# Kernel tuning notes

Measured on AMD Instinct MI355X. Metric: run time of the kernel, lower is better.

Reference implementation:

```python
import jax, jax.numpy as jnp
import numpy as np

VOCAB = 32000
EMBED = 512
HIDDEN = 1024
MAX_VOCAB = 33000
MAX_LEN = 128
BATCH = 64


def setup_inputs() -> dict:
    key = jax.random.key(0)
    ks = jax.random.split(key, 20)
    s = 0.02
    H, E, L, V = HIDDEN, EMBED, MAX_LEN, VOCAB
    return {
        "input_tok": jax.random.randint(ks[0], (BATCH,), 0, V, dtype=jnp.int64 if jax.config.jax_enable_x64 else jnp.int32),
        "hidden": jax.random.normal(ks[1], (1, BATCH, H), jnp.float32),
        "encoder_outputs": jax.random.normal(ks[2], (BATCH, L, H), jnp.float32),
        "input_seq": jax.random.randint(ks[3], (BATCH, L), 0, V, dtype=jnp.int64 if jax.config.jax_enable_x64 else jnp.int32),
        "pre_prob": jax.random.uniform(ks[4], (BATCH, L), jnp.float32),
        "emb": jax.random.normal(ks[5], (V, E), jnp.float32) * s,
        "attn_W": jax.random.normal(ks[6], (L, H + E), jnp.float32) * s,
        "attn_b": jnp.zeros((L,), jnp.float32),
        "comb_W": jax.random.normal(ks[7], (H, H + E), jnp.float32) * s,
        "comb_b": jnp.zeros((H,), jnp.float32),
        "W_ih": jax.random.normal(ks[8], (3 * H, 2 * H), jnp.float32) * s,
        "W_hh": jax.random.normal(ks[9], (3 * H, H), jnp.float32) * s,
        "b_ih": jnp.zeros((3 * H,), jnp.float32),
        "b_hh": jnp.zeros((3 * H,), jnp.float32),
        "Wo_W": jax.random.normal(ks[10], (V, H), jnp.float32) * s,
        "Wo_b": jnp.zeros((V,), jnp.float32),
        "Wc_W": jax.random.normal(ks[11], (H, H), jnp.float32) * s,
        "Wc_b": jnp.zeros((H,), jnp.float32),
    }


def _decoder_step(input_tok, hidden, encoder_outputs, input_seq, pre_prob,
                  emb, attn_W, attn_b, comb_W, comb_b,
                  W_ih, W_hh, b_ih, b_hh, Wo_W, Wo_b, Wc_W, Wc_b):
    B = encoder_outputs.shape[0]
    H = hidden.shape[-1]
    V = Wo_W.shape[0]
    # selective read: mask where previous output token matches source tokens
    sel = (input_tok[:, None] == input_seq).astype(pre_prob.dtype) * pre_prob  # [B,L]
    # torch does encoder_outputs.long().float() -> truncation toward zero
    sel_reading = jnp.einsum('bl,blh->bh', sel, jnp.trunc(encoder_outputs))  # [B,H]

    embedded = emb[input_tok]  # [B,E] (dropout is identity in eval)
    h = hidden[0]  # [B,H]

    a = jnp.concatenate([embedded, h], axis=1) @ attn_W.T + attn_b  # [B,L]
    attn_weights = jax.nn.softmax(a, axis=1)
    attn_applied = jnp.einsum('bl,blh->bh', attn_weights, encoder_outputs)  # [B,H]

    out = jnp.concatenate([embedded, attn_applied], axis=1) @ comb_W.T + comb_b
    out = jax.nn.relu(out)  # [B,H]

    gru_in = jnp.concatenate([out, sel_reading], axis=1)  # [B,2H]
    gi = gru_in @ W_ih.T + b_ih  # [B,3H]
    gh = h @ W_hh.T + b_hh       # [B,3H]
    i_r, i_z, i_n = jnp.split(gi, 3, axis=1)
    h_r, h_z, h_n = jnp.split(gh, 3, axis=1)
    r = jax.nn.sigmoid(i_r + h_r)
    z = jax.nn.sigmoid(i_z + h_z)
    n = jnp.tanh(i_n + r * h_n)
    h_new = (1.0 - z) * n + z * h  # [B,H]

    score_g = h_new @ Wo_W.T + Wo_b  # [B,V]
    score_c = jnp.tanh(encoder_outputs @ Wc_W.T + Wc_b)  # [B,L,H]
    score_c = jnp.einsum('blh,bh->bl', score_c, h_new)   # [B,L]

    score = jax.nn.softmax(jnp.concatenate([score_g, score_c], axis=1), axis=1)
    prob_g = score[:, :V]
    prob_c = score[:, V:]  # [B,L]

    output1 = jnp.concatenate(
        [prob_g, jnp.zeros((B, MAX_VOCAB - V), prob_g.dtype)], axis=1)  # [B,MAX_VOCAB]
    # bmm(prob_c, one_hot(input_seq)) == scatter-add of copy probs onto vocab ids
    b_idx = jnp.arange(B)[:, None]
    output1 = output1.at[b_idx, input_seq].add(prob_c)
    output1 = jnp.where(output1 == 0, 1e-9, output1)
    output1 = output1.at[:, 2].set(1e-9)
    output1 = jnp.log(output1)
    return output1, h_new[None], attn_weights, prob_c


def reference(input_tok, hidden, encoder_outputs, input_seq, pre_prob,
              emb, attn_W, attn_b, comb_W, comb_b,
              W_ih, W_hh, b_ih, b_hh, Wo_W, Wo_b, Wc_W, Wc_b):
    return _decoder_step(input_tok, hidden, encoder_outputs, input_seq, pre_prob,
                         emb, attn_W, attn_b, comb_W, comb_b,
                         W_ih, W_hh, b_ih, b_hh, Wo_W, Wo_b, Wc_W, Wc_b)
```

## Files before the change

kernel.cpp:

```cpp
#include <hip/hip_runtime.h>
#include <math.h>

#define BB 64
#define LL 128
#define HH 1024
#define EE 512
#define VV 32000
#define MAXV 33000

typedef float f32x4 __attribute__((ext_vector_type(4)));
typedef short bf16x8 __attribute__((ext_vector_type(8)));
typedef unsigned u32x4 __attribute__((ext_vector_type(4)));

__device__ __forceinline__ void gload_lds16(const void* g, void* l) {
    __builtin_amdgcn_global_load_lds((const __attribute__((address_space(1))) void*)g,
                                     (__attribute__((address_space(3))) void*)l, 16, 0, 0);
}

__device__ __forceinline__ unsigned short f2bf(float f) {
    unsigned u = __float_as_uint(f);
    return (unsigned short)((u + 0x7fffu + ((u >> 16) & 1u)) >> 16);
}

__device__ __forceinline__ unsigned pkbf(float a, float b) {
    unsigned r;
    asm("v_cvt_pk_bf16_f32 %0, %1, %2" : "=v"(r) : "v"(a), "v"(b));
    return r;
}

__device__ __forceinline__ float fexp(float x) { return __expf(x); }
__device__ __forceinline__ float flog(float x) { return __logf(x); }
__device__ __forceinline__ float ftanh(float x) { return 1.f - 2.f / (1.f + __expf(2.f * x)); }

__device__ __forceinline__ void smerge(float& m, float& s, float m2, float s2) {
    float nm = fmaxf(m, m2);
    s = s * fexp(m - nm) + s2 * fexp(m2 - nm);
    m = nm;
}

#define N_ENC4 2097152
__global__ void setup2(const float* __restrict__ enc, unsigned short* __restrict__ encB,
                       const float* __restrict__ WcW, unsigned short* __restrict__ WcB,
                       const int* __restrict__ tok, const float* __restrict__ hidden,
                       const float* __restrict__ emb, unsigned short* __restrict__ xaB,
                       const float* __restrict__ attnb, const float* __restrict__ combb,
                       const float* __restrict__ bih, const float* __restrict__ bhh,
                       float* __restrict__ aT, float* __restrict__ gruOutF,
                       float* __restrict__ giT, float* __restrict__ ghT,
                       float* __restrict__ zeros, float* __restrict__ out1) {
    int idx = blockIdx.x * 256 + threadIdx.x;
    if (idx < N_ENC4) {
        float4 v = ((const float4*)enc)[idx];
        ushort4 o;
        o.x = f2bf(v.x); o.y = f2bf(v.y); o.z = f2bf(v.z); o.w = f2bf(v.w);
        ((ushort4*)encB)[idx] = o;
        return;
    }
    idx -= N_ENC4;
    if (idx < 262144) {
        float4 v = ((const float4*)WcW)[idx];
        ushort4 o;
        o.x = f2bf(v.x); o.y = f2bf(v.y); o.z = f2bf(v.z); o.w = f2bf(v.w);
        ((ushort4*)WcB)[idx] = o;
        return;
    }
    idx -= 262144;
    if (idx < 98304) {
        int b = idx / 1536, k = idx % 1536;
        float v = (k < EE) ? emb[tok[b] * EE + k] : hidden[b * HH + (k - EE)];
        xaB[b * 1536 + k] = f2bf(v);
        return;
    }
    idx -= 98304;
    if (idx < 8192) { aT[idx] = attnb[idx >> 6]; return; }
    idx -= 8192;
    if (idx < 65536) { gruOutF[idx] = combb[idx >> 6]; return; }
    idx -= 65536;
    if (idx < 196608) { giT[idx] = bih[idx >> 6]; return; }
    idx -= 196608;
    if (idx < 196608) { ghT[idx] = bhh[idx >> 6]; return; }
    idx -= 196608;
    if (idx < 139264) { zeros[idx] = 0.f; return; }
    idx -= 139264;
    int b = idx / 8000, q = idx % 8000;
    ((float4*)(out1 + (size_t)b * MAXV))[q] = (float4){0.f, 0.f, 0.f, 0.f};
}

template <int DIRECT, int MI>
__device__ __forceinline__ void mgemm_body(int bid,
        const float* __restrict__ W, const float* __restrict__ bias,
        const unsigned short* __restrict__ xA, int sA,
        const unsigned short* __restrict__ xB, int sB, int K1,
        int K, int Kc, int splitk, float* __restrict__ out) {
    int tid = threadIdx.x, w = tid >> 6, lane = tid & 63;
    int rb = bid / splitk, kseg = bid - rb * splitk;
    int r0 = rb * (MI * 64), kb0 = kseg * Kc;
    int lr = lane & 15, lk = lane >> 4;
    int nt = Kc >> 6;
    f32x4 acc[MI][4];
#pragma unroll
    for (int mi = 0; mi < MI; ++mi)
#pragma unroll
        for (int nf = 0; nf < 4; ++nf) acc[mi][nf] = (f32x4){0.f, 0.f, 0.f, 0.f};
    const float* Wr[MI];
#pragma unroll
    for (int mi = 0; mi < MI; ++mi)
        Wr[mi] = W + (size_t)(r0 + w * (MI * 16) + mi * 16 + lr) * K;

    for (int t = 0; t < nt; ++t) {
        int kb = kb0 + t * 64;
        bf16x8 bfr[2][4];
#pragma unroll
        for (int ks = 0; ks < 2; ++ks)
#pragma unroll
            for (int nf = 0; nf < 4; ++nf) {
                int bcol = nf * 16 + lr;
                int kg = kb + ks * 32 + lk * 8;
                const unsigned short* xp = (kg < K1) ? (xA + bcol * sA + kg)
                                                     : (xB + bcol * sB + (kg - K1));
                bfr[ks][nf] = *(const bf16x8*)xp;
            }
        bf16x8 afr[MI][2];
#pragma unroll
        for (int mi = 0; mi < MI; ++mi)
#pragma unroll
            for (int ks = 0; ks < 2; ++ks) {
                const float* wp = Wr[mi] + kb + ks * 32 + lk * 8;
                float4 w0 = *(const float4*)wp;
                float4 w1 = *(const float4*)(wp + 4);
                union { u32x4 u; bf16x8 h; } cv;
                cv.u[0] = pkbf(w0.x, w0.y); cv.u[1] = pkbf(w0.z, w0.w);
                cv.u[2] = pkbf(w1.x, w1.y); cv.u[3] = pkbf(w1.z, w1.w);
                afr[mi][ks] = cv.h;
            }
#pragma unroll
        for (int ks = 0; ks < 2; ++ks)
#pragma unroll
            for (int mi = 0; mi < MI; ++mi)
#pragma unroll
                for (int nf = 0; nf < 4; ++nf)
                    acc[mi][nf] = __builtin_amdgcn_mfma_f32_16x16x32_bf16(
                        afr[mi][ks], bfr[ks][nf], acc[mi][nf], 0, 0, 0);
    }
#pragma unroll
    for (int mi = 0; mi < MI; ++mi)
#pragma unroll
        for (int nf = 0; nf < 4; ++nf)
#pragma unroll
            for (int reg = 0; reg < 4; ++reg) {
                int r = r0 + w * (MI * 16) + mi * 16 + lk * 4 + reg;
                int bcol = nf * 16 + lr;
                float v = acc[mi][nf][reg];
                if (DIRECT) out[r * 64 + bcol] = v + bias[r];
                else atomicAdd(&out[r * 64 + bcol], v);
            }
}

template <int DIRECT, int MI>
__global__ __launch_bounds__(256) void mgemm(
        const float* __restrict__ W, const float* __restrict__ bias,
        const unsigned short* __restrict__ xA, int sA,
        const unsigned short* __restrict__ xB, int sB, int K1,
        int K, int Kc, int splitk, float* __restrict__ out) {
    mgemm_body<DIRECT, MI>(blockIdx.x, W, bias, xA, sA, xB, sB, K1, K, Kc, splitk, out);
}

__global__ __launch_bounds__(256) void gru2(
        const float* __restrict__ Wih, const float* __restrict__ Whh,
        const unsigned short* __restrict__ gruInB, const unsigned short* __restrict__ xaB512,
        float* __restrict__ giT, float* __restrict__ ghT) {
    const float* W; const unsigned short* x; int s, K1, K, Kc; float* out; int bid;
    if (blockIdx.x < 192) { W = Wih; x = gruInB; s = 2048; K1 = 2048; K = 2048; Kc = 256; out = giT; bid = blockIdx.x; }
    else                  { W = Whh; x = xaB512; s = 1536; K1 = 1024; K = 1024; Kc = 128; out = ghT; bid = blockIdx.x - 192; }
    mgemm_body<0, 2>(bid, W, nullptr, x, s, x, s, K1, K, Kc, 8, out);
}

__global__ __launch_bounds__(256) void k2_softmax_enc(
        const float* __restrict__ aT, const int* __restrict__ tok, const int* __restrict__ seq,
        const float* __restrict__ pprob, const float* __restrict__ enc,
        float* __restrict__ ap4T, float* __restrict__ gruSelF, float* __restrict__ out3) {
    int b = blockIdx.x, lc = blockIdx.y, t = threadIdx.x;
    __shared__ float red[256];
    __shared__ float w_s[16], sel_s[16];
    float av = (t < LL) ? aT[t * 64 + b] : -1e30f;
    red[t] = av; __syncthreads();
    for (int s = 128; s > 0; s >>= 1) { if (t < s) red[t] = fmaxf(red[t], red[t + s]); __syncthreads(); }
    float m = red[0]; __syncthreads();
    float e = (t < LL) ? fexp(av - m) : 0.f;
    red[t] = e; __syncthreads();
    for (int s = 128; s > 0; s >>= 1) { if (t < s) red[t] += red[t + s]; __syncthreads(); }
    float Z = red[0]; __syncthreads();
    if (t < LL) {
        float wv = e / Z;
        if (lc == 0) out3[b * LL + t] = wv;
        int l0 = lc * 16;
        if (t >= l0 && t < l0 + 16) {
            w_s[t - l0] = wv;
            sel_s[t - l0] = (seq[b * LL + t] == tok[b]) ? pprob[b * LL + t] : 0.f;
        }
    }
    __syncthreads();
    float accA[4] = {0.f,0.f,0.f,0.f}, accS[4] = {0.f,0.f,0.f,0.f};
    const float* encb = enc + (size_t)b * LL * HH + (size_t)lc * 16 * HH;
    for (int l = 0; l < 16; ++l) {
        float wl = w_s[l], sl = sel_s[l];
#pragma unroll
        for (int i = 0; i < 4; ++i) {
            float ev = encb[l * HH + t + i * 256];
            accA[i] += wl * ev;
            accS[i] += sl * truncf(ev);
        }
    }
#pragma unroll
    for (int i = 0; i < 4; ++i) {
        int h = t + i * 256;
        atomicAdd(&ap4T[(h >> 2) * 256 + b * 4 + (h & 3)], accA[i]);
        atomicAdd(&gruSelF[(h >> 2) * 256 + b * 4 + (h & 3)], accS[i]);
    }
}

__global__ void cvt_ap(const float* __restrict__ ap4T, unsigned short* __restrict__ apB) {
    int tid = blockIdx.x * 256 + threadIdx.x;
    int b = tid & 63, kq = tid >> 6;
    float4 v = *(const float4*)&ap4T[kq * 256 + b * 4];
    ushort4 o;
    o.x = f2bf(v.x); o.y = f2bf(v.y); o.z = f2bf(v.z); o.w = f2bf(v.w);
    *(ushort4*)&apB[b * 1024 + kq * 4] = o;
}

__global__ void cvt_gruIn(const float* __restrict__ gruOutF, const float* __restrict__ gruSelF,
                          unsigned short* __restrict__ gruInB) {
    int tid = blockIdx.x * 256 + threadIdx.x;
    int b = tid & 63, kq = tid >> 6;
    float4 v;
    if (kq < 256) {
        int k = kq * 4;
        v.x = fmaxf(gruOutF[(k + 0) * 64 + b], 0.f);
        v.y = fmaxf(gruOutF[(k + 1) * 64 + b], 0.f);
        v.z = fmaxf(gruOutF[(k + 2) * 64 + b], 0.f);
        v.w = fmaxf(gruOutF[(k + 3) * 64 + b], 0.f);
    } else {
        v = *(const float4*)&gruSelF[(kq - 256) * 256 + b * 4];
    }
    ushort4 o;
    o.x = f2bf(v.x); o.y = f2bf(v.y); o.z = f2bf(v.z); o.w = f2bf(v.w);
    *(ushort4*)&gruInB[b * 2048 + kq * 4] = o;
}

__global__ void k5_gates(const float* __restrict__ giT, const float* __restrict__ ghT,
                         const float* __restrict__ hidden, float* __restrict__ hn4T,
                         unsigned short* __restrict__ hnB, float* __restrict__ out2) {
    int idx = blockIdx.x * 256 + threadIdx.x;
    int r = idx >> 6, b = idx & 63;
    float ir = giT[r * 64 + b], iz = giT[(HH + r) * 64 + b], in_ = giT[(2 * HH + r) * 64 + b];
    float hr = ghT[r * 64 + b], hz = ghT[(HH + r) * 64 + b], hn = ghT[(2 * HH + r) * 64 + b];
    float rr = 1.f / (1.f + fexp(-(ir + hr)));
    float zz = 1.f / (1.f + fexp(-(iz + hz)));
    float nn = ftanh(in_ + rr * hn);
    float hprev = hidden[b * HH + r];
    float hnew = (1.f - zz) * nn + zz * hprev;
    hn4T[(r >> 2) * 256 + b * 4 + (r & 3)] = hnew;
    hnB[b * 1024 + r] = f2bf(hnew);
    out2[b * HH + r] = hnew;
}

__global__ __launch_bounds__(256) void wow_f1(
        const float* __restrict__ WoW, const float* __restrict__ Wob,
        const unsigned short* __restrict__ hnB, float* __restrict__ sgT,
        float* __restrict__ partMt, float* __restrict__ partSt) {
    __shared__ float pm_s[4 * 64], ps_s[4 * 64];
    int tid = threadIdx.x, w = tid >> 6, lane = tid & 63;
    int lr = lane & 15, lk = lane >> 4;
    int r0 = blockIdx.x * 64;
    f32x4 acc[4];
#pragma unroll
    for (int nf = 0; nf < 4; ++nf) acc[nf] = (f32x4){0.f, 0.f, 0.f, 0.f};
    const float* Wr = WoW + (size_t)(r0 + w * 16 + lr) * HH;
    for (int t = 0; t < 16; ++t) {
        int kb = t * 64;
        bf16x8 bfr[2][4];
#pragma unroll
        for (int ks = 0; ks < 2; ++ks)
#pragma unroll
            for (int nf = 0; nf < 4; ++nf)
                bfr[ks][nf] = *(const bf16x8*)(hnB + (nf * 16 + lr) * 1024 + kb + ks * 32 + lk * 8);
        bf16x8 afr[2];
#pragma unroll
        for (int ks = 0; ks < 2; ++ks) {
            const float* wp = Wr + kb + ks * 32 + lk * 8;
            float4 w0 = *(const float4*)wp;
            float4 w1 = *(const float4*)(wp + 4);
            union { u32x4 u; bf16x8 h; } cv;
            cv.u[0] = pkbf(w0.x, w0.y); cv.u[1] = pkbf(w0.z, w0.w);
            cv.u[2] = pkbf(w1.x, w1.y); cv.u[3] = pkbf(w1.z, w1.w);
            afr[ks] = cv.h;
        }
#pragma unroll
        for (int ks = 0; ks < 2; ++ks)
#pragma unroll
            for (int nf = 0; nf < 4; ++nf)
                acc[nf] = __builtin_amdgcn_mfma_f32_16x16x32_bf16(afr[ks], bfr[ks][nf], acc[nf], 0, 0, 0);
    }
#pragma unroll
    for (int nf = 0; nf < 4; ++nf) {
        int bcol = nf * 16 + lr;
        float m = -1e30f, s = 0.f;
#pragma unroll
        for (int reg = 0; reg < 4; ++reg) {
            int r = r0 + w * 16 + lk * 4 + reg;
            float v = acc[nf][reg] + Wob[r];
            sgT[r * 64 + bcol] = v;
            float nm = fmaxf(m, v);
            s = s * fexp(m - nm) + fexp(v - nm);
            m = nm;
        }
#pragma unroll
        for (int d = 16; d <= 32; d <<= 1) {
            float om = __shfl_xor(m, d), os = __shfl_xor(s, d);
            smerge(m, s, om, os);
        }
        if (lk == 0) { pm_s[w * 64 + bcol] = m; ps_s[w * 64 + bcol] = s; }
    }
    __syncthreads();
    if (tid < 64) {
        float m = pm_s[tid], s = ps_s[tid];
        smerge(m, s, pm_s[64 + tid], ps_s[64 + tid]);
        smerge(m, s, pm_s[128 + tid], ps_s[128 + tid]);
        smerge(m, s, pm_s[192 + tid], ps_s[192 + tid]);
        partMt[tid * 512 + blockIdx.x] = m;
        partSt[tid * 512 + blockIdx.x] = s;
    }
}

__global__ __launch_bounds__(256) void k7_mfma(const unsigned short* __restrict__ encB,
        const unsigned short* __restrict__ WcB, const float* __restrict__ Wcb,
        const float* __restrict__ hn4T, float* __restrict__ sc) {
    __shared__ __align__(16) unsigned short As[128 * 64];
    __shared__ __align__(16) unsigned short Bs[128 * 64];
    __shared__ float h_s[128], bias_s[128];
    int tid = threadIdx.x, w = tid >> 6, lane = tid & 63;
    int wm = w >> 1, wn = w & 1;
    int bid = blockIdx.x;
    int swz = (bid & 7) * 64 + (bid >> 3);
    int mt = swz >> 3, nt = swz & 7;
    int m0 = mt * 128, n0 = nt * 128;
    if (tid < 128) {
        int n = n0 + tid;
        bias_s[tid] = Wcb[n];
        h_s[tid] = hn4T[(n >> 2) * 256 + mt * 4 + (n & 3)];
    }
    f32x4 acc[4][4];
#pragma unroll
    for (int mi = 0; mi < 4; ++mi)
#pragma unroll
        for (int ni = 0; ni < 4; ++ni) acc[mi][ni] = (f32x4){0.f, 0.f, 0.f, 0.f};

    for (int kt = 0; kt < 16; ++kt) {
        __syncthreads();
#pragma unroll
        for (int i = 0; i < 4; ++i) {
            int c = i * 256 + tid;
            int row = c >> 3, cc = c & 7;
            int lc2 = cc ^ (row & 7);
            gload_lds16(encB + (size_t)(m0 + row) * HH + kt * 64 + lc2 * 8,
                        (char*)As + (i * 256 + w * 64) * 16);
        }
#pragma unroll
        for (int i = 0; i < 4; ++i) {
            int c = i * 256 + tid;
            int row = c >> 3, cc = c & 7;
            int lc2 = cc ^ (row & 7);
            gload_lds16(WcB + (size_t)(n0 + row) * HH + kt * 64 + lc2 * 8,
                        (char*)Bs + (i * 256 + w * 64) * 16);
        }
        asm volatile("s_waitcnt vmcnt(0)");
        __syncthreads();
#pragma unroll
        for (int ks = 0; ks < 2; ++ks) {
            bf16x8 af[4], bf[4];
#pragma unroll
            for (int mi = 0; mi < 4; ++mi) {
                int rr = wm * 64 + mi * 16 + (lane & 15);
                int lkk = ks * 4 + (lane >> 4);
                af[mi] = *(const bf16x8*)((const char*)As + rr * 128 + ((lkk ^ (rr & 7)) * 16));
            }
#pragma unroll
            for (int ni = 0; ni < 4; ++ni) {
                int rr = wn * 64 + ni * 16 + (lane & 15);
                int lkk = ks * 4 + (lane >> 4);
                bf[ni] = *(const bf16x8*)((const char*)Bs + rr * 128 + ((lkk ^ (rr & 7)) * 16));
            }
#pragma unroll
            for (int mi = 0; mi < 4; ++mi)
#pragma unroll
                for (int ni = 0; ni < 4; ++ni)
                    acc[mi][ni] = __builtin_amdgcn_mfma_f32_16x16x32_bf16(af[mi], bf[ni], acc[mi][ni], 0, 0, 0);
        }
    }
    float rs[16];
#pragma unroll
    for (int z = 0; z < 16; ++z) rs[z] = 0.f;
#pragma unroll
    for (int ni = 0; ni < 4; ++ni) {
        int nl = wn * 64 + ni * 16 + (lane & 15);
        float hv = h_s[nl], bv = bias_s[nl];
#pragma unroll
        for (int mi = 0; mi < 4; ++mi)
#pragma unroll
            for (int reg = 0; reg < 4; ++reg)
                rs[mi * 4 + reg] += ftanh(acc[mi][ni][reg] + bv) * hv;
    }
#pragma unroll
    for (int z = 0; z < 16; ++z) {
        float v = rs[z];
        v += __shfl_xor(v, 1); v += __shfl_xor(v, 2);
        v += __shfl_xor(v, 4); v += __shfl_xor(v, 8);
        rs[z] = v;
    }
    if ((lane & 15) == 0) {
        int g = lane >> 4;
#pragma unroll
        for (int mi = 0; mi < 4; ++mi)
#pragma unroll
            for (int reg = 0; reg < 4; ++reg)
                atomicAdd(&sc[mt * LL + wm * 64 + mi * 16 + g * 4 + reg], rs[mi * 4 + reg]);
    }
}

__global__ __launch_bounds__(256) void f1c_final(const float* __restrict__ partMt,
        const float* __restrict__ partSt, const float* __restrict__ sc,
        const int* __restrict__ seq, float* __restrict__ Mb, float* __restrict__ Zb,
        float* __restrict__ out4, float* __restrict__ out1) {
    int b = blockIdx.x, t = threadIdx.x;
    __shared__ float mred[256], sred[256];
    float m = -1e30f, s = 0.f;
    for (int w = t; w < 500; w += 256)
        smerge(m, s, partMt[b * 512 + w], partSt[b * 512 + w]);
    if (t < 128) smerge(m, s, sc[b * LL + t], 1.0f);
    mred[t] = m; sred[t] = s; __syncthreads();
    for (int st = 128; st > 0; st >>= 1) {
        if (t < st) {
            float mm = mred[t], ss = sred[t];
            smerge(mm, ss, mred[t + st], sred[t + st]);
            mred[t] = mm; sred[t] = ss;
        }
        __syncthreads();
    }
    float M = mred[0], Z = sred[0];
    if (t == 0) { Mb[b] = M; Zb[b] = Z; }
    if (t < 128) {
        float p = fexp(sc[b * LL + t] - M) / Z;
        out4[b * LL + t] = p;
        atomicAdd(&out1[(size_t)b * MAXV + seq[b * LL + t]], p);
    }
}

__global__ void f2f4_final(const float* __restrict__ sgT, const float* __restrict__ Mb,
                           const float* __restrict__ Zb, float* __restrict__ out1) {
    int b = blockIdx.y;
    int v = blockIdx.x * 256 + threadIdx.x;
    if (v >= MAXV) return;
    float val = 0.f;
    if (v < VV) {
        float scat = out1[(size_t)b * MAXV + v];
        val = fexp(sgT[v * 64 + b] - Mb[b]) / Zb[b] + scat;
    }
    if (v == 2 || val == 0.f) val = 1e-9f;
    out1[(size_t)b * MAXV + v] = flog(val);
}

extern "C" void kernel_launch(void* const* d_in, const int* in_sizes, int n_in,
                              void* d_out, int out_size, void* d_ws, size_t ws_size,
                              hipStream_t stream) {
    (void)in_sizes; (void)n_in; (void)out_size; (void)ws_size;
    const int*   tok    = (const int*)  d_in[0];
    const float* hidden = (const float*)d_in[1];
    const float* enc    = (const float*)d_in[2];
    const int*   seq    = (const int*)  d_in[3];
    const float* pprob  = (const float*)d_in[4];
    const float* emb    = (const float*)d_in[5];
    const float* attnW  = (const float*)d_in[6];
    const float* attnb  = (const float*)d_in[7];
    const float* combW  = (const float*)d_in[8];
    const float* combb  = (const float*)d_in[9];
    const float* Wih    = (const float*)d_in[10];
    const float* Whh    = (const float*)d_in[11];
    const float* bih    = (const float*)d_in[12];
    const float* bhh    = (const float*)d_in[13];
    const float* WoW    = (const float*)d_in[14];
    const float* Wob    = (const float*)d_in[15];
    const float* WcW    = (const float*)d_in[16];
    const float* Wcb    = (const float*)d_in[17];

    float* out1 = (float*)d_out;
    float* out2 = out1 + (size_t)BB * MAXV;
    float* out3 = out2 + BB * HH;
    float* out4 = out3 + BB * LL;

    float* ws      = (float*)d_ws;
    float* aT      = ws;
    float* ap4T    = ws + 8192;
    float* gruSelF = ws + 73728;
    float* sc      = ws + 139264;
    float* gruOutF = ws + 147456;
    float* giT     = ws + 212992;
    float* ghT     = ws + 409600;
    float* hn4T    = ws + 606208;
    float* sgT     = ws + 671744;
    float* partMt  = ws + 2719744;
    float* partSt  = ws + 2752512;
    float* Mb      = ws + 2785280;
    float* Zb      = ws + 2785344;
    unsigned short* encB = (unsigned short*)(ws + 2785408);
    unsigned short* WcB  = encB + 8388608;
    unsigned short* hnB  = (unsigned short*)(ws + 7504000);
    unsigned short* xaB    = (unsigned short*)sgT;
    unsigned short* apB    = (unsigned short*)(ws + 720896);
    unsigned short* gruInB = (unsigned short*)(ws + 753664);

    setup2       <<<13968, 256, 0, stream>>>(enc, encB, WcW, WcB, tok, hidden, emb, xaB,
                                             attnb, combb, bih, bhh,
                                             aT, gruOutF, giT, ghT, ap4T, out1);
    mgemm<0,2>   <<<12, 256, 0, stream>>>(attnW, nullptr, xaB, 1536, xaB, 1536, 1536, 1536, 128, 12, aT);
    k2_softmax_enc<<<dim3(64, 8), 256, 0, stream>>>(aT, tok, seq, pprob, enc, ap4T, gruSelF, out3);
    cvt_ap       <<<64, 256, 0, stream>>>(ap4T, apB);
    mgemm<0,2>   <<<96, 256, 0, stream>>>(combW, nullptr, xaB, 1536, apB, 1024, 512, 1536, 128, 12, gruOutF);
    cvt_gruIn    <<<128, 256, 0, stream>>>(gruOutF, gruSelF, gruInB);
    gru2         <<<384, 256, 0, stream>>>(Wih, Whh, gruInB, xaB + 512, giT, ghT);
    k5_gates     <<<256, 256, 0, stream>>>(giT, ghT, hidden, hn4T, hnB, out2);
    wow_f1       <<<500, 256, 0, stream>>>(WoW, Wob, hnB, sgT, partMt, partSt);
    k7_mfma      <<<512, 256, 0, stream>>>(encB, WcB, Wcb, hn4T, sc);
    f1c_final    <<<64, 256, 0, stream>>>(partMt, partSt, sc, seq, Mb, Zb, out4, out1);
    f2f4_final   <<<dim3(129, 64), 256, 0, stream>>>(sgT, Mb, Zb, out1);
}
```

Baseline: 174.4 us.

## Split Wo GEMM K across warps and double block count with register prefetch

The vocab-projection kernel now gives each block 32 rows instead of 64. Its four warps are split into two row groups by two K halves, and the K-half partials are reduced through shared memory. That doubles the grid to 1000 blocks. The loop also prefetches the next fp32 weight chunk into registers before converting and issuing MFMAs, to hide global-load latency on the 131 MB weight stream. The cost is an extra LDS reduction, twice as many softmax partials for the final kernel to merge, and a shifted workspace layout.

Result: slower. 179.9 us (+3.2%).

```diff
diff --git a/kernel.cpp b/kernel.cpp
--- a/kernel.cpp
+++ b/kernel.cpp
@@ -268,67 +268,84 @@
         const float* __restrict__ WoW, const float* __restrict__ Wob,
         const unsigned short* __restrict__ hnB, float* __restrict__ sgT,
         float* __restrict__ partMt, float* __restrict__ partSt) {
-    __shared__ float pm_s[4 * 64], ps_s[4 * 64];
+    __shared__ float red_s[32 * 64];
+    __shared__ float pm_s[2 * 64], ps_s[2 * 64];
     int tid = threadIdx.x, w = tid >> 6, lane = tid & 63;
     int lr = lane & 15, lk = lane >> 4;
-    int r0 = blockIdx.x * 64;
+    int wr = w & 1, wk = w >> 1;
+    int r0 = blockIdx.x * 32;
+    const float* Wr = WoW + (size_t)(r0 + wr * 16 + lr) * HH + wk * 512;
     f32x4 acc[4];
 #pragma unroll
     for (int nf = 0; nf < 4; ++nf) acc[nf] = (f32x4){0.f, 0.f, 0.f, 0.f};
-    const float* Wr = WoW + (size_t)(r0 + w * 16 + lr) * HH;
-    for (int t = 0; t < 16; ++t) {
+    float4 pA0 = *(const float4*)(Wr + lk * 8);
+    float4 pA1 = *(const float4*)(Wr + lk * 8 + 4);
+    float4 pB0 = *(const float4*)(Wr + 32 + lk * 8);
+    float4 pB1 = *(const float4*)(Wr + 32 + lk * 8 + 4);
+    for (int t = 0; t < 8; ++t) {
         int kb = t * 64;
         bf16x8 bfr[2][4];
 #pragma unroll
         for (int ks = 0; ks < 2; ++ks)
 #pragma unroll
             for (int nf = 0; nf < 4; ++nf)
-                bfr[ks][nf] = *(const bf16x8*)(hnB + (nf * 16 + lr) * 1024 + kb + ks * 32 + lk * 8);
-        bf16x8 afr[2];
-#pragma unroll
-        for (int ks = 0; ks < 2; ++ks) {
-            const float* wp = Wr + kb + ks * 32 + lk * 8;
-            float4 w0 = *(const float4*)wp;
-            float4 w1 = *(const float4*)(wp + 4);
-            union { u32x4 u; bf16x8 h; } cv;
-            cv.u[0] = pkbf(w0.x, w0.y); cv.u[1] = pkbf(w0.z, w0.w);
-            cv.u[2] = pkbf(w1.x, w1.y); cv.u[3] = pkbf(w1.z, w1.w);
-            afr[ks] = cv.h;
-        }
-#pragma unroll
-        for (int ks = 0; ks < 2; ++ks)
-#pragma unroll
-            for (int nf = 0; nf < 4; ++nf)
-                acc[nf] = __builtin_amdgcn_mfma_f32_16x16x32_bf16(afr[ks], bfr[ks][nf], acc[nf], 0, 0, 0);
-    }
-#pragma unroll
-    for (int nf = 0; nf < 4; ++nf) {
-        int bcol = nf * 16 + lr;
-        float m = -1e30f, s = 0.f;
-#pragma unroll
-        for (int reg = 0; reg < 4; ++reg) {
-            int r = r0 + w * 16 + lk * 4 + reg;
-            float v = acc[nf][reg] + Wob[r];
-            sgT[r * 64 + bcol] = v;
-            float nm = fmaxf(m, v);
-            s = s * fexp(m - nm) + fexp(v - nm);
-            m = nm;
-        }
-#pragma unroll
-        for (int d = 16; d <= 32; d <<= 1) {
-            float om = __shfl_xor(m, d), os = __shfl_xor(s, d);
-            smerge(m, s, om, os);
-        }
-        if (lk == 0) { pm_s[w * 64 + bcol] = m; ps_s[w * 64 + bcol] = s; }
+                bfr[ks][nf] = *(const bf16x8*)(hnB + (nf * 16 + lr) * 1024 + wk * 512 + kb + ks * 32 + lk * 8);
+        float4 cA0 = pA0, cA1 = pA1, cB0 = pB0, cB1 = pB1;
+        if (t < 7) {
+            const float* wn = Wr + (t + 1) * 64 + lk * 8;
+            pA0 = *(const float4*)(wn);
+            pA1 = *(const float4*)(wn + 4);
+            pB0 = *(const float4*)(wn + 32);
+            pB1 = *(const float4*)(wn + 36);
+        }
+        union { u32x4 u; bf16x8 h; } c0, c1;
+        c0.u[0] = pkbf(cA0.x, cA0.y); c0.u[1] = pkbf(cA0.z, cA0.w);
+        c0.u[2] = pkbf(cA1.x, cA1.y); c0.u[3] = pkbf(cA1.z, cA1.w);
+        c1.u[0] = pkbf(cB0.x, cB0.y); c1.u[1] = pkbf(cB0.z, cB0.w);
+        c1.u[2] = pkbf(cB1.x, cB1.y); c1.u[3] = pkbf(cB1.z, cB1.w);
+#pragma unroll
+        for (int nf = 0; nf < 4; ++nf) {
+            acc[nf] = __builtin_amdgcn_mfma_f32_16x16x32_bf16(c0.h, bfr[0][nf], acc[nf], 0, 0, 0);
+            acc[nf] = __builtin_amdgcn_mfma_f32_16x16x32_bf16(c1.h, bfr[1][nf], acc[nf], 0, 0, 0);
+        }
+    }
+    if (wk == 1) {
+#pragma unroll
+        for (int nf = 0; nf < 4; ++nf)
+#pragma unroll
+            for (int reg = 0; reg < 4; ++reg)
+                red_s[(wr * 16 + lk * 4 + reg) * 64 + nf * 16 + lr] = acc[nf][reg];
+    }
+    __syncthreads();
+    if (wk == 0) {
+#pragma unroll
+        for (int nf = 0; nf < 4; ++nf) {
+            int bcol = nf * 16 + lr;
+            float m = -1e30f, s = 0.f;
+#pragma unroll
+            for (int reg = 0; reg < 4; ++reg) {
+                int rloc = wr * 16 + lk * 4 + reg;
+                int r = r0 + rloc;
+                float v = acc[nf][reg] + red_s[rloc * 64 + bcol] + Wob[r];
+                sgT[r * 64 + bcol] = v;
+                float nm = fmaxf(m, v);
+                s = s * fexp(m - nm) + fexp(v - nm);
+                m = nm;
+            }
+#pragma unroll
+            for (int d = 16; d <= 32; d <<= 1) {
+                float om = __shfl_xor(m, d), os = __shfl_xor(s, d);
+                smerge(m, s, om, os);
+            }
+            if (lk == 0) { pm_s[wr * 64 + bcol] = m; ps_s[wr * 64 + bcol] = s; }
+        }
     }
     __syncthreads();
     if (tid < 64) {
         float m = pm_s[tid], s = ps_s[tid];
         smerge(m, s, pm_s[64 + tid], ps_s[64 + tid]);
-        smerge(m, s, pm_s[128 + tid], ps_s[128 + tid]);
-        smerge(m, s, pm_s[192 + tid], ps_s[192 + tid]);
-        partMt[tid * 512 + blockIdx.x] = m;
-        partSt[tid * 512 + blockIdx.x] = s;
+        partMt[tid * 1024 + blockIdx.x] = m;
+        partSt[tid * 1024 + blockIdx.x] = s;
     }
 }
 
@@ -434,8 +451,8 @@
     int b = blockIdx.x, t = threadIdx.x;
     __shared__ float mred[256], sred[256];
     float m = -1e30f, s = 0.f;
-    for (int w = t; w < 500; w += 256)
-        smerge(m, s, partMt[b * 512 + w], partSt[b * 512 + w]);
+    for (int w = t; w < 1000; w += 256)
+        smerge(m, s, partMt[b * 1024 + w], partSt[b * 1024 + w]);
     if (t < 128) smerge(m, s, sc[b * LL + t], 1.0f);
     mred[t] = m; sred[t] = s; __syncthreads();
     for (int st = 128; st > 0; st >>= 1) {
@@ -508,12 +525,12 @@
     float* hn4T    = ws + 606208;
     float* sgT     = ws + 671744;
     float* partMt  = ws + 2719744;
-    float* partSt  = ws + 2752512;
-    float* Mb      = ws + 2785280;
-    float* Zb      = ws + 2785344;
-    unsigned short* encB = (unsigned short*)(ws + 2785408);
+    float* partSt  = ws + 2785280;
+    float* Mb      = ws + 2850816;
+    float* Zb      = ws + 2850880;
+    unsigned short* encB = (unsigned short*)(ws + 2850944);
     unsigned short* WcB  = encB + 8388608;
-    unsigned short* hnB  = (unsigned short*)(ws + 7504000);
+    unsigned short* hnB  = (unsigned short*)(ws + 7569536);
     unsigned short* xaB    = (unsigned short*)sgT;
     unsigned short* apB    = (unsigned short*)(ws + 720896);
     unsigned short* gruInB = (unsigned short*)(ws + 753664);
@@ -528,7 +545,7 @@
     cvt_gruIn    <<<128, 256, 0, stream>>>(gruOutF, gruSelF, gruInB);
     gru2         <<<384, 256, 0, stream>>>(Wih, Whh, gruInB, xaB + 512, giT, ghT);
     k5_gates     <<<256, 256, 0, stream>>>(giT, ghT, hidden, hn4T, hnB, out2);
-    wow_f1       <<<500, 256, 0, stream>>>(WoW, Wob, hnB, sgT, partMt, partSt);
+    wow_f1       <<<1000, 256, 0, stream>>>(WoW, Wob, hnB, sgT, partMt, partSt);
     k7_mfma      <<<512, 256, 0, stream>>>(encB, WcB, Wcb, hn4T, sc);
     f1c_final    <<<64, 256, 0, stream>>>(partMt, partSt, sc, seq, Mb, Zb, out4, out1);
     f2f4_final   <<<dim3(129, 64), 256, 0, stream>>>(sgT, Mb, Zb, out1);
```
